# Kernel optimization log

Hardware: AMD Instinct MI355X
Metric: run time of the kernel (lower is better)

## Reference

```python
import jax, jax.numpy as jnp
import numpy as np

B = 1024        # batch
S = 2048        # nsampled + 1 (index 0 is the positive label)
E = 128         # emb_size
V = 100000      # vocab = len(tags_weight)


def setup_inputs() -> dict:
    key = jax.random.key(0)
    k1, k2, k3, k4 = jax.random.split(key, 4)
    inputs = jax.random.normal(k1, (B, E), dtype=jnp.float32)
    weight = jax.random.normal(k2, (V, E), dtype=jnp.float32)
    bias = jax.random.normal(k3, (V,), dtype=jnp.float32)
    sample_ids = jax.random.randint(k4, (B, S), 0, V)  # column 0 = positive label
    return {"inputs": inputs, "weight": weight, "bias": bias, "sample_ids": sample_ids}


def reference(inputs, weight, bias, sample_ids):
    # Gather sampled rows: [B, S, E] and [B, S]
    sample_weights = weight[sample_ids]
    sample_bias = bias[sample_ids]
    # Batched dot: logits[b, s] = <inputs[b], sample_weights[b, s]> + bias
    logits = jnp.einsum('be,bse->bs', inputs, sample_weights) + sample_bias
    # CrossEntropyLoss with targets all-zero (positive class is at index 0), mean reduction
    loss = jnp.mean(jax.nn.logsumexp(logits, axis=-1) - logits[:, 0])
    return loss
```

## Files before the change

### kernel.cpp

```cpp
#include <hip/hip_runtime.h>
#include <float.h>
#include <math.h>

#define BATCH 1024
#define NS    2048
#define EMB   128
#define VOCAB 100000
#define THREADS 256
#define CHUNKS 4
#define SCHUNK (NS / CHUNKS)
#define ITERS  (SCHUNK / 64)

typedef float floatx2 __attribute__((ext_vector_type(2)));

#if __has_builtin(__builtin_amdgcn_cvt_pk_f32_fp8) && __has_builtin(__builtin_amdgcn_cvt_pk_fp8_f32)
#define USE_FP8_BUILTINS 1
#else
#define USE_FP8_BUILTINS 0
#include <hip/hip_fp8.h>
#endif

__device__ inline floatx2 cvt2_lo(unsigned int w) {
#if USE_FP8_BUILTINS
    return __builtin_amdgcn_cvt_pk_f32_fp8((int)w, false);
#else
    __hip_fp8_e4m3 a, b;
    a.__x = (unsigned char)(w & 0xff);
    b.__x = (unsigned char)((w >> 8) & 0xff);
    floatx2 r; r.x = (float)a; r.y = (float)b; return r;
#endif
}
__device__ inline floatx2 cvt2_hi(unsigned int w) {
#if USE_FP8_BUILTINS
    return __builtin_amdgcn_cvt_pk_f32_fp8((int)w, true);
#else
    __hip_fp8_e4m3 a, b;
    a.__x = (unsigned char)((w >> 16) & 0xff);
    b.__x = (unsigned char)((w >> 24) & 0xff);
    floatx2 r; r.x = (float)a; r.y = (float)b; return r;
#endif
}
__device__ inline unsigned int pack4_fp8(float4 v) {
#if USE_FP8_BUILTINS
    int w = 0;
    w = __builtin_amdgcn_cvt_pk_fp8_f32(v.x, v.y, w, false);
    w = __builtin_amdgcn_cvt_pk_fp8_f32(v.z, v.w, w, true);
    return (unsigned int)w;
#else
    __hip_fp8_e4m3 h0(v.x), h1(v.y), h2(v.z), h3(v.w);
    return (unsigned int)h0.__x | ((unsigned int)h1.__x << 8)
         | ((unsigned int)h2.__x << 16) | ((unsigned int)h3.__x << 24);
#endif
}

__global__ __launch_bounds__(THREADS) void convert_weights_fp8(
    const float* __restrict__ w, unsigned int* __restrict__ w8)
{
    const size_t i = (size_t)blockIdx.x * THREADS + threadIdx.x;
    const float4* src = (const float4*)w;
    float4 a = src[4 * i + 0];
    float4 b = src[4 * i + 1];
    float4 c = src[4 * i + 2];
    float4 d = src[4 * i + 3];
    uint4 o;
    o.x = pack4_fp8(a);
    o.y = pack4_fp8(b);
    o.z = pack4_fp8(c);
    o.w = pack4_fp8(d);
    ((uint4*)w8)[i] = o;
}

__global__ __launch_bounds__(THREADS) void sampled_ce_partial_8(
    const float*        __restrict__ inputs,
    const unsigned int* __restrict__ w8,
    const float*        __restrict__ bias,
    const int*          __restrict__ sample_ids,
    float* __restrict__ pm,
    float* __restrict__ pl,
    float* __restrict__ plogit0)
{
    const int blk   = blockIdx.x;
    const int b     = blk >> 2;
    const int chunk = blk & (CHUNKS - 1);
    const int t = threadIdx.x;
    const int e_part  = t & 3;
    const int s_local = t >> 2;

    __shared__ float s_in[EMB];
    __shared__ float s_red[8];

    if (t < EMB / 4) {
        ((float4*)s_in)[t] = ((const float4*)(inputs + (size_t)b * EMB))[t];
    }

    const int* ids_row = sample_ids + (size_t)b * NS + chunk * SCHUNK;
    int ids[ITERS];
#pragma unroll
    for (int it = 0; it < ITERS; ++it) ids[it] = ids_row[it * 64 + s_local];
    float bv[ITERS];
#pragma unroll
    for (int it = 0; it < ITERS; ++it) bv[it] = bias[ids[it]];

    __syncthreads();

    floatx2 cin[2][8];
#pragma unroll
    for (int k = 0; k < 2; ++k)
#pragma unroll
        for (int p = 0; p < 8; ++p) {
            const int base = k * 64 + e_part * 16 + 2 * p;
            cin[k][p].x = s_in[base];
            cin[k][p].y = s_in[base + 1];
        }

    float m = -FLT_MAX;
    float l = 0.0f;

#pragma unroll
    for (int it = 0; it < ITERS; ++it) {
        const uint4* wr = (const uint4*)(w8 + (size_t)ids[it] * (EMB / 4));
        floatx2 acc2 = {0.0f, 0.0f};
#pragma unroll
        for (int k = 0; k < 2; ++k) {
            uint4 q = wr[k * 4 + e_part];
            acc2 += cvt2_lo(q.x) * cin[k][0];
            acc2 += cvt2_hi(q.x) * cin[k][1];
            acc2 += cvt2_lo(q.y) * cin[k][2];
            acc2 += cvt2_hi(q.y) * cin[k][3];
            acc2 += cvt2_lo(q.z) * cin[k][4];
            acc2 += cvt2_hi(q.z) * cin[k][5];
            acc2 += cvt2_lo(q.w) * cin[k][6];
            acc2 += cvt2_hi(q.w) * cin[k][7];
        }
        float acc = acc2.x + acc2.y;
        acc += __shfl_xor(acc, 1, 64);
        acc += __shfl_xor(acc, 2, 64);
        const float logit = acc + bv[it];

        const float nm = fmaxf(m, logit);
        l = l * __expf(m - nm) + __expf(logit - nm);
        m = nm;

        if (chunk == 0 && it == 0 && t == 0) plogit0[b] = logit;
    }

    if (e_part != 0) { m = -FLT_MAX; l = 0.0f; }

#pragma unroll
    for (int off = 1; off < 64; off <<= 1) {
        const float om = __shfl_xor(m, off, 64);
        const float ol = __shfl_xor(l, off, 64);
        const float nm = fmaxf(m, om);
        l = l * __expf(m - nm) + ol * __expf(om - nm);
        m = nm;
    }

    const int wave = t >> 6;
    if ((t & 63) == 0) { s_red[wave * 2] = m; s_red[wave * 2 + 1] = l; }
    __syncthreads();

    if (t == 0) {
        float M = s_red[0], L = s_red[1];
#pragma unroll
        for (int w = 1; w < 4; ++w) {
            const float om = s_red[w * 2], ol = s_red[w * 2 + 1];
            const float nm = fmaxf(M, om);
            L = L * __expf(M - nm) + ol * __expf(om - nm);
            M = nm;
        }
        pm[blk] = M;
        pl[blk] = L;
    }
}

__global__ __launch_bounds__(THREADS) void sampled_ce_partial_f(
    const float* __restrict__ inputs,
    const float* __restrict__ weight,
    const float* __restrict__ bias,
    const int*   __restrict__ sample_ids,
    float* __restrict__ pm,
    float* __restrict__ pl,
    float* __restrict__ plogit0)
{
    const int blk   = blockIdx.x;
    const int b     = blk >> 2;
    const int chunk = blk & (CHUNKS - 1);
    const int t = threadIdx.x;
    const int e_part  = t & 3;
    const int s_local = t >> 2;

    __shared__ float s_in[EMB];
    __shared__ float s_red[8];

    if (t < EMB / 4) {
        ((float4*)s_in)[t] = ((const float4*)(inputs + (size_t)b * EMB))[t];
    }
    const int* ids_row = sample_ids + (size_t)b * NS + chunk * SCHUNK;
    int ids[ITERS];
#pragma unroll
    for (int it = 0; it < ITERS; ++it) ids[it] = ids_row[it * 64 + s_local];

    __syncthreads();

    float4 cin[8];
#pragma unroll
    for (int k = 0; k < 8; ++k) cin[k] = ((const float4*)s_in)[k * 4 + e_part];

    float m = -FLT_MAX;
    float l = 0.0f;

#pragma unroll
    for (int it = 0; it < ITERS; ++it) {
        const int id = ids[it];
        const float4* wr = (const float4*)(weight + (size_t)id * EMB);
        float acc = 0.0f;
#pragma unroll
        for (int k = 0; k < 8; ++k) {
            float4 w = wr[k * 4 + e_part];
            acc += w.x * cin[k].x + w.y * cin[k].y + w.z * cin[k].z + w.w * cin[k].w;
        }
        acc += __shfl_xor(acc, 1, 64);
        acc += __shfl_xor(acc, 2, 64);
        const float logit = acc + bias[id];
        const float nm = fmaxf(m, logit);
        l = l * __expf(m - nm) + __expf(logit - nm);
        m = nm;
        if (chunk == 0 && it == 0 && t == 0) plogit0[b] = logit;
    }

    if (e_part != 0) { m = -FLT_MAX; l = 0.0f; }
#pragma unroll
    for (int off = 1; off < 64; off <<= 1) {
        const float om = __shfl_xor(m, off, 64);
        const float ol = __shfl_xor(l, off, 64);
        const float nm = fmaxf(m, om);
        l = l * __expf(m - nm) + ol * __expf(om - nm);
        m = nm;
    }
    const int wave = t >> 6;
    if ((t & 63) == 0) { s_red[wave * 2] = m; s_red[wave * 2 + 1] = l; }
    __syncthreads();
    if (t == 0) {
        float M = s_red[0], L = s_red[1];
#pragma unroll
        for (int w = 1; w < 4; ++w) {
            const float om = s_red[w * 2], ol = s_red[w * 2 + 1];
            const float nm = fmaxf(M, om);
            L = L * __expf(M - nm) + ol * __expf(om - nm);
            M = nm;
        }
        pm[blk] = M;
        pl[blk] = L;
    }
}

__global__ __launch_bounds__(1024) void sampled_ce_finalize(
    const float* __restrict__ pm,
    const float* __restrict__ pl,
    const float* __restrict__ plogit0,
    float* __restrict__ out)
{
    const int t = threadIdx.x;

    float M = pm[t * CHUNKS + 0];
    float L = pl[t * CHUNKS + 0];
#pragma unroll
    for (int c = 1; c < CHUNKS; ++c) {
        const float om = pm[t * CHUNKS + c];
        const float ol = pl[t * CHUNKS + c];
        const float nm = fmaxf(M, om);
        L = L * __expf(M - nm) + ol * __expf(om - nm);
        M = nm;
    }
    float v = (M + __logf(L) - plogit0[t]) * (1.0f / (float)BATCH);

#pragma unroll
    for (int off = 1; off < 64; off <<= 1) v += __shfl_xor(v, off, 64);

    __shared__ float s[16];
    if ((t & 63) == 0) s[t >> 6] = v;
    __syncthreads();

    if (t == 0) {
        float sum = 0.0f;
#pragma unroll
        for (int w = 0; w < 16; ++w) sum += s[w];
        out[0] = sum;
    }
}

extern "C" void kernel_launch(void* const* d_in, const int* in_sizes, int n_in,
                              void* d_out, int out_size, void* d_ws, size_t ws_size,
                              hipStream_t stream) {
    const float* inputs     = (const float*)d_in[0];
    const float* weight     = (const float*)d_in[1];
    const float* bias       = (const float*)d_in[2];
    const int*   sample_ids = (const int*)d_in[3];
    float* out = (float*)d_out;

    float* ws = (float*)d_ws;
    float* pm      = ws;
    float* pl      = ws + BATCH * CHUNKS;
    float* plogit0 = ws + 2 * BATCH * CHUNKS;
    const size_t red_bytes = (size_t)(2 * BATCH * CHUNKS + BATCH) * sizeof(float);
    const size_t w8_bytes  = (size_t)VOCAB * EMB;
    unsigned int* w8 = (unsigned int*)((char*)d_ws + red_bytes);

    if (ws_size >= red_bytes + w8_bytes) {
        convert_weights_fp8<<<dim3((VOCAB * EMB) / (16 * THREADS)), dim3(THREADS), 0, stream>>>(
            weight, w8);
        sampled_ce_partial_8<<<dim3(BATCH * CHUNKS), dim3(THREADS), 0, stream>>>(
            inputs, w8, bias, sample_ids, pm, pl, plogit0);
    } else {
        sampled_ce_partial_f<<<dim3(BATCH * CHUNKS), dim3(THREADS), 0, stream>>>(
            inputs, weight, bias, sample_ids, pm, pl, plogit0);
    }

    sampled_ce_finalize<<<dim3(1), dim3(1024), 0, stream>>>(pm, pl, plogit0, out);
}
```

Baseline: 133.9 us.

## Prefetch all fp8 weight rows up front with 8-lane split and 8 chunks

The fp8 partial kernel now splits each batch row into 8 chunks and uses 8 lanes per sample, each loading one 16-byte fp8 segment. Sample ids are staged through shared memory, and all weight rows and biases for a thread are issued as loads before any compute. This raises memory-level parallelism for the random gather. The online softmax is replaced by a two-pass max then sum over register-held logits, and a launch-bounds occupancy hint is added. Costs are more registers, twice as many blocks and partials to reduce, and an extra shuffle step per sample.

```diff
diff --git a/kernel.cpp b/kernel.cpp
--- a/kernel.cpp
+++ b/kernel.cpp
@@ -7,9 +7,10 @@
 #define EMB   128
 #define VOCAB 100000
 #define THREADS 256
-#define CHUNKS 4
+#define CHUNKS 8
 #define SCHUNK (NS / CHUNKS)
-#define ITERS  (SCHUNK / 64)
+#define ITERS8 (SCHUNK / 32)
+#define ITERSF (SCHUNK / 64)
 
 typedef float floatx2 __attribute__((ext_vector_type(2)));
 
@@ -70,7 +71,7 @@
     ((uint4*)w8)[i] = o;
 }
 
-__global__ __launch_bounds__(THREADS) void sampled_ce_partial_8(
+__global__ __launch_bounds__(THREADS, 4) void sampled_ce_partial_8(
     const float*        __restrict__ inputs,
     const unsigned int* __restrict__ w8,
     const float*        __restrict__ bias,
@@ -80,69 +81,74 @@
     float* __restrict__ plogit0)
 {
     const int blk   = blockIdx.x;
-    const int b     = blk >> 2;
+    const int b     = blk >> 3;
     const int chunk = blk & (CHUNKS - 1);
     const int t = threadIdx.x;
-    const int e_part  = t & 3;
-    const int s_local = t >> 2;
+    const int e_part = t & 7;
+    const int s_sub  = t >> 3;
 
     __shared__ float s_in[EMB];
+    __shared__ int   s_ids[SCHUNK];
     __shared__ float s_red[8];
+
+    const int* ids_row = sample_ids + (size_t)b * NS + chunk * SCHUNK;
 
     if (t < EMB / 4) {
         ((float4*)s_in)[t] = ((const float4*)(inputs + (size_t)b * EMB))[t];
     }
-
-    const int* ids_row = sample_ids + (size_t)b * NS + chunk * SCHUNK;
-    int ids[ITERS];
-#pragma unroll
-    for (int it = 0; it < ITERS; ++it) ids[it] = ids_row[it * 64 + s_local];
-    float bv[ITERS];
-#pragma unroll
-    for (int it = 0; it < ITERS; ++it) bv[it] = bias[ids[it]];
-
-    __syncthreads();
-
-    floatx2 cin[2][8];
-#pragma unroll
-    for (int k = 0; k < 2; ++k)
-#pragma unroll
-        for (int p = 0; p < 8; ++p) {
-            const int base = k * 64 + e_part * 16 + 2 * p;
-            cin[k][p].x = s_in[base];
-            cin[k][p].y = s_in[base + 1];
-        }
-
-    float m = -FLT_MAX;
-    float l = 0.0f;
-
-#pragma unroll
-    for (int it = 0; it < ITERS; ++it) {
-        const uint4* wr = (const uint4*)(w8 + (size_t)ids[it] * (EMB / 4));
+    if (t >= 64 && t < 64 + SCHUNK / 4) {
+        ((int4*)s_ids)[t - 64] = ((const int4*)ids_row)[t - 64];
+    }
+    __syncthreads();
+
+    int ids[ITERS8];
+#pragma unroll
+    for (int it = 0; it < ITERS8; ++it) ids[it] = s_ids[it * 32 + s_sub];
+
+    uint4 q[ITERS8];
+#pragma unroll
+    for (int it = 0; it < ITERS8; ++it) {
+        q[it] = ((const uint4*)w8)[(size_t)ids[it] * 8 + e_part];
+    }
+    float bv[ITERS8];
+#pragma unroll
+    for (int it = 0; it < ITERS8; ++it) bv[it] = bias[ids[it]];
+
+    floatx2 cin[8];
+#pragma unroll
+    for (int p = 0; p < 8; ++p) {
+        const int base = e_part * 16 + 2 * p;
+        cin[p].x = s_in[base];
+        cin[p].y = s_in[base + 1];
+    }
+
+    float logits[ITERS8];
+#pragma unroll
+    for (int it = 0; it < ITERS8; ++it) {
         floatx2 acc2 = {0.0f, 0.0f};
-#pragma unroll
-        for (int k = 0; k < 2; ++k) {
-            uint4 q = wr[k * 4 + e_part];
-            acc2 += cvt2_lo(q.x) * cin[k][0];
-            acc2 += cvt2_hi(q.x) * cin[k][1];
-            acc2 += cvt2_lo(q.y) * cin[k][2];
-            acc2 += cvt2_hi(q.y) * cin[k][3];
-            acc2 += cvt2_lo(q.z) * cin[k][4];
-            acc2 += cvt2_hi(q.z) * cin[k][5];
-            acc2 += cvt2_lo(q.w) * cin[k][6];
-            acc2 += cvt2_hi(q.w) * cin[k][7];
-        }
+        acc2 += cvt2_lo(q[it].x) * cin[0];
+        acc2 += cvt2_hi(q[it].x) * cin[1];
+        acc2 += cvt2_lo(q[it].y) * cin[2];
+        acc2 += cvt2_hi(q[it].y) * cin[3];
+        acc2 += cvt2_lo(q[it].z) * cin[4];
+        acc2 += cvt2_hi(q[it].z) * cin[5];
+        acc2 += cvt2_lo(q[it].w) * cin[6];
+        acc2 += cvt2_hi(q[it].w) * cin[7];
         float acc = acc2.x + acc2.y;
         acc += __shfl_xor(acc, 1, 64);
         acc += __shfl_xor(acc, 2, 64);
-        const float logit = acc + bv[it];
-
-        const float nm = fmaxf(m, logit);
-        l = l * __expf(m - nm) + __expf(logit - nm);
-        m = nm;
-
-        if (chunk == 0 && it == 0 && t == 0) plogit0[b] = logit;
-    }
+        acc += __shfl_xor(acc, 4, 64);
+        logits[it] = acc + bv[it];
+    }
+
+    if (chunk == 0 && t == 0) plogit0[b] = logits[0];
+
+    float m = logits[0];
+#pragma unroll
+    for (int it = 1; it < ITERS8; ++it) m = fmaxf(m, logits[it]);
+    float l = 0.0f;
+#pragma unroll
+    for (int it = 0; it < ITERS8; ++it) l += __expf(logits[it] - m);
 
     if (e_part != 0) { m = -FLT_MAX; l = 0.0f; }
 
@@ -183,7 +189,7 @@
     float* __restrict__ plogit0)
 {
     const int blk   = blockIdx.x;
-    const int b     = blk >> 2;
+    const int b     = blk >> 3;
     const int chunk = blk & (CHUNKS - 1);
     const int t = threadIdx.x;
     const int e_part  = t & 3;
@@ -196,9 +202,9 @@
         ((float4*)s_in)[t] = ((const float4*)(inputs + (size_t)b * EMB))[t];
     }
     const int* ids_row = sample_ids + (size_t)b * NS + chunk * SCHUNK;
-    int ids[ITERS];
-#pragma unroll
-    for (int it = 0; it < ITERS; ++it) ids[it] = ids_row[it * 64 + s_local];
+    int ids[ITERSF];
+#pragma unroll
+    for (int it = 0; it < ITERSF; ++it) ids[it] = ids_row[it * 64 + s_local];
 
     __syncthreads();
 
@@ -210,7 +216,7 @@
     float l = 0.0f;
 
 #pragma unroll
-    for (int it = 0; it < ITERS; ++it) {
+    for (int it = 0; it < ITERSF; ++it) {
         const int id = ids[it];
         const float4* wr = (const float4*)(weight + (size_t)id * EMB);
         float acc = 0.0f;
```

Result: faster. 128.1 us (-4.4%).
